# Performance work log

Hardware: AMD Instinct MI355X
Metric: run time of the kernel (lower is better)

The kernel has to match this reference:

```python
import jax, jax.numpy as jnp
import numpy as np

NUM_HEADS = 12

def setup_inputs() -> dict:
    key = jax.random.key(0)
    ks = jax.random.split(key, 6)
    B, N, C = 4, 2048, 768
    s = 0.02
    return {
        "x": jax.random.normal(ks[0], (B, N, C), jnp.float32),
        "y": jax.random.normal(ks[1], (B, N, C), jnp.float32),
        "Wq": jax.random.normal(ks[2], (C, C), jnp.float32) * s,
        "Wkv": jax.random.normal(ks[3], (2 * C, C), jnp.float32) * s,
        "tau_param": jnp.asarray(1.0, jnp.float32),
        "Wproj": jax.random.normal(ks[4], (C, C), jnp.float32) * s,
        "bproj": jnp.zeros((C,), jnp.float32),
    }

def reference(x, y, Wq, Wkv, tau_param, Wproj, bproj):
    B, N, C = x.shape
    H = NUM_HEADS
    D = C // H
    scale = D ** -0.5
    # q: [B,H,N,D]
    q = (x @ Wq.T).reshape(B, N, H, D).transpose(0, 2, 1, 3) * scale
    kv = (y @ Wkv.T).reshape(B, N, 2, H, D).transpose(2, 0, 3, 1, 4)
    k, v = kv[0], kv[1]
    tau = jax.nn.softplus(tau_param) + 1e-6
    attn = jnp.einsum("bhnd,bhmd->bhnm", q, k) / tau  # [B,H,N,N]
    attn = jax.nn.softmax(attn, axis=-1)
    out = jnp.einsum("bhnm,bhmd->bhnd", attn, v)  # [B,H,N,D]
    out = out.transpose(0, 2, 1, 3).reshape(B, N, C)
    return out @ Wproj.T + bproj
```

## Files before the change

### kernel.cpp

```cpp
#include <hip/hip_runtime.h>
#include <math.h>

typedef unsigned short u16;
typedef unsigned int u32;
typedef __fp16 fp16x2 __attribute__((ext_vector_type(2)));
typedef _Float16 half8 __attribute__((ext_vector_type(8)));
typedef float f32x4 __attribute__((ext_vector_type(4)));

#define NH   12
#define SEQ  2048
#define CDIM 768

__device__ __forceinline__ u16 f2h(float f) {
  _Float16 h = (_Float16)f;
  return __builtin_bit_cast(u16, h);
}
__device__ __forceinline__ u32 pk2(float a, float b) {
  fp16x2 h = __builtin_amdgcn_cvt_pkrtz(a, b);
  return __builtin_bit_cast(u32, h);
}
__device__ __forceinline__ void dma16(const u16* g, u16* l) {
  __builtin_amdgcn_global_load_lds(
      (const __attribute__((address_space(1))) u32*)g,
      (__attribute__((address_space(3))) u32*)l, 16, 0, 0);
}

__global__ __launch_bounds__(256) void cvt_xy(const float* __restrict__ x,
                                              const float* __restrict__ y,
                                              u16* __restrict__ xh, u16* __restrict__ yh) {
  const long NEL = 8192l * 768;
  long i = ((long)blockIdx.x * 256 + threadIdx.x) * 4;
  const float* in = (i < NEL) ? x : y;
  u16* out = (i < NEL) ? xh : yh;
  long j = (i < NEL) ? i : i - NEL;
  float4 f = *(const float4*)(in + j);
  *(uint2*)(out + j) = make_uint2(pk2(f.x, f.y), pk2(f.z, f.w));
}
__global__ __launch_bounds__(256) void cvt_w(const float* __restrict__ Wq,
                                             const float* __restrict__ Wkv,
                                             const float* __restrict__ Wp,
                                             const float* __restrict__ taup,
                                             u16* __restrict__ wqh, u16* __restrict__ wkh,
                                             u16* __restrict__ wph) {
  const long E1 = 768l * 768, E2 = E1 + 1536l * 768;
  long i = ((long)blockIdx.x * 256 + threadIdx.x) * 4;
  const float* in; u16* out; long j; float s;
  if (i < E1) {
    float t = *taup;
    float sp = (t > 20.f) ? t : log1pf(expf(t));
    s = (0.125f / (sp + 1e-6f)) * 1.44269504088896340736f;
    in = Wq; out = wqh; j = i;
  } else if (i < E2) {
    s = 1.f; in = Wkv; out = wkh; j = i - E1;
  } else {
    s = 1.f; in = Wp; out = wph; j = i - E2;
  }
  float4 f = *(const float4*)(in + j);
  *(uint2*)(out + j) = make_uint2(pk2(f.x * s, f.y * s), pk2(f.z * s, f.w * s));
}

template<int MODE, int BN, int WPB>
__global__ __launch_bounds__(256, WPB) void gemm_k(
    const u16* __restrict__ A0, const u16* __restrict__ A1,
    const u16* __restrict__ B0, const u16* __restrict__ B1,
    u16* __restrict__ oq, u16* __restrict__ ok, u16* __restrict__ ovt,
    float* __restrict__ outf, const float* __restrict__ bias)
{
  constexpr int NT = BN / 32;
  __shared__ __align__(16) u16 As[2][128 * 64];
  __shared__ __align__(16) u16 Bs[2][BN * 64];
  const int tid = threadIdx.x;
  const int wave = tid >> 6, lane = tid & 63;
  const int quad = lane >> 4, l16 = lane & 15;
  const int wr = wave >> 1, wc = wave & 1;
  const int row0 = blockIdx.x * 128;
  const int by = blockIdx.y;

  const u16* A; const u16* Bm; int cb;
  if (MODE == 0) {
    if (by < 6) { A = A0; Bm = B0; cb = by; }
    else        { A = A1; Bm = B1; cb = by - 6; }
  } else {
    A = A0; Bm = B0; cb = by;
  }
  const int col0 = cb * BN;

  const int sub = lane >> 3;
  const int csw = ((lane & 7) ^ sub) * 8;

  f32x4 acc[4][NT] = {};

  auto stage = [&](int k0, int bsel) {
    #pragma unroll
    for (int i = 0; i < 4; i++) {
      int ii = wave * 4 + i;
      dma16(A + (size_t)(row0 + ii * 8 + sub) * 768 + k0 + csw, &As[bsel][ii * 512]);
    }
    #pragma unroll
    for (int i = 0; i < BN / 32; i++) {
      int ii = wave * (BN / 32) + i;
      dma16(Bm + (size_t)(col0 + ii * 8 + sub) * 768 + k0 + csw, &Bs[bsel][ii * 512]);
    }
  };

  stage(0, 0);
  __syncthreads();

  #pragma unroll 1
  for (int t = 0; t < 12; t++) {
    const int cur = t & 1;
    if (t + 1 < 12) stage((t + 1) << 6, cur ^ 1);
    const u16* Asp = As[cur];
    const u16* Bsp = Bs[cur];
    #pragma unroll
    for (int ks = 0; ks < 2; ks++) {
      half8 af[4], bfr[NT];
      #pragma unroll
      for (int mt = 0; mt < 4; mt++)
        af[mt] = *(const half8*)&Asp[(wr * 64 + mt * 16 + l16) * 64 + (((ks * 4 + quad) ^ (l16 & 7)) * 8)];
      #pragma unroll
      for (int nt = 0; nt < NT; nt++)
        bfr[nt] = *(const half8*)&Bsp[(wc * (BN / 2) + nt * 16 + l16) * 64 + (((ks * 4 + quad) ^ (l16 & 7)) * 8)];
      #pragma unroll
      for (int mt = 0; mt < 4; mt++)
        #pragma unroll
        for (int nt = 0; nt < NT; nt++)
          acc[mt][nt] = __builtin_amdgcn_mfma_f32_16x16x32_f16(af[mt], bfr[nt], acc[mt][nt], 0, 0, 0);
    }
    __syncthreads();
  }

  #pragma unroll
  for (int mt = 0; mt < 4; mt++)
  #pragma unroll
  for (int nt = 0; nt < NT; nt++) {
    int gm0 = row0 + wr * 64 + mt * 16 + quad * 4;
    int gn = col0 + wc * (BN / 2) + nt * 16 + l16;
    f32x4 v = acc[mt][nt];
    if (MODE == 0) {
      int b = gm0 >> 11, n0 = gm0 & 2047;
      if (by < 6) {
        int h = gn >> 6, d = gn & 63;
        size_t base = (((size_t)(b * NH + h)) * SEQ + n0) * 64 + d;
        #pragma unroll
        for (int r = 0; r < 4; r++) oq[base + (size_t)r * 64] = f2h(v[r]);
      } else if (gn < CDIM) {
        int h = gn >> 6, d = gn & 63;
        size_t base = (((size_t)(b * NH + h)) * SEQ + n0) * 64 + d;
        #pragma unroll
        for (int r = 0; r < 4; r++) ok[base + (size_t)r * 64] = f2h(v[r]);
      } else {
        int c = gn - CDIM;
        int h = c >> 6, d = c & 63;
        *(uint2*)&ovt[(((size_t)(b * NH + h)) * 64 + d) * SEQ + n0] =
            make_uint2(pk2(v[0], v[1]), pk2(v[2], v[3]));
      }
    } else {
      float bv = bias[gn];
      #pragma unroll
      for (int r = 0; r < 4; r++)
        outf[(size_t)(gm0 + r) * CDIM + gn] = v[r] + bv;
    }
  }
}

__global__ __launch_bounds__(256, 3) void attn_kernel(
    const u16* __restrict__ Q, const u16* __restrict__ Kb,
    const u16* __restrict__ Vtg, u16* __restrict__ Ob)
{
  __shared__ __align__(16) u16 Ks[2][64 * 64];
  __shared__ __align__(16) u16 Vs[2][64 * 64];
  __shared__ __align__(16) u16 Ps[4 * 16 * 64];

  const int bid = (blockIdx.x & 7) * 96 + (blockIdx.x >> 3);
  const int qt = bid & 15;
  const int bh = bid >> 4;
  const int b = bh / NH, h = bh % NH;
  const u16* Qp = Q   + (size_t)bh * SEQ * 64;
  const u16* Kp = Kb  + (size_t)bh * SEQ * 64;
  const u16* Vp = Vtg + (size_t)bh * 64 * SEQ;

  const int tid = threadIdx.x;
  const int wave = tid >> 6, lane = tid & 63;
  const int quad = lane >> 4, l16 = lane & 15;
  const int sub = lane >> 3;
  const int csw = ((lane & 7) ^ sub) * 8;
  u16* Pw = Ps + wave * 16 * 64;

  half8 vone;
  #pragma unroll
  for (int j = 0; j < 8; j++) vone[j] = (_Float16)1.0f;

  half8 qf[2][2];
  #pragma unroll
  for (int mt = 0; mt < 2; mt++)
    #pragma unroll
    for (int ks = 0; ks < 2; ks++)
      qf[mt][ks] = *(const half8*)(Qp + (size_t)(qt * 128 + wave * 32 + mt * 16 + l16) * 64 + ks * 32 + quad * 8);

  f32x4 oacc[2][4] = {};
  f32x4 lacc[2] = {};

  auto stage = [&](int kt, int bsel) {
    #pragma unroll
    for (int i = 0; i < 2; i++) {
      int ii = wave * 2 + i;
      dma16(Kp + (size_t)(kt * 64 + ii * 8 + sub) * 64 + csw, &Ks[bsel][ii * 512]);
      dma16(Vp + (size_t)(ii * 8 + sub) * SEQ + kt * 64 + csw, &Vs[bsel][ii * 512]);
    }
  };

  stage(0, 0);
  __syncthreads();

  for (int kt = 0; kt < SEQ / 64; kt++) {
    const int cur = kt & 1;
    if (kt + 1 < SEQ / 64) stage(kt + 1, cur ^ 1);
    const u16* Ksp = Ks[cur];
    const u16* Vsp = Vs[cur];

    f32x4 sacc[2][4] = {};
    __builtin_amdgcn_s_setprio(1);
    #pragma unroll
    for (int ks = 0; ks < 2; ks++) {
      #pragma unroll
      for (int ntk = 0; ntk < 4; ntk++) {
        half8 kf = *(const half8*)&Ksp[(ntk * 16 + l16) * 64 + (((ks * 4 + quad) ^ (l16 & 7)) * 8)];
        #pragma unroll
        for (int mt = 0; mt < 2; mt++)
          sacc[mt][ntk] = __builtin_amdgcn_mfma_f32_16x16x32_f16(kf, qf[mt][ks], sacc[mt][ntk], 0, 0, 0);
      }
    }
    __builtin_amdgcn_s_setprio(0);

    half8 pf[2][2];
    #pragma unroll
    for (int mt = 0; mt < 2; mt++) {
      #pragma unroll
      for (int ntk = 0; ntk < 4; ntk++) {
        float p0 = __builtin_amdgcn_exp2f(sacc[mt][ntk][0]);
        float p1 = __builtin_amdgcn_exp2f(sacc[mt][ntk][1]);
        float p2 = __builtin_amdgcn_exp2f(sacc[mt][ntk][2]);
        float p3 = __builtin_amdgcn_exp2f(sacc[mt][ntk][3]);
        *(uint2*)&Pw[l16 * 64 + (((ntk * 2 + (quad >> 1)) ^ (l16 & 7)) * 8) + (quad & 1) * 4] =
            make_uint2(pk2(p0, p1), pk2(p2, p3));
      }
      pf[mt][0] = *(const half8*)&Pw[l16 * 64 + ((quad ^ (l16 & 7)) * 8)];
      pf[mt][1] = *(const half8*)&Pw[l16 * 64 + (((4 + quad) ^ (l16 & 7)) * 8)];
    }

    __builtin_amdgcn_s_setprio(1);
    #pragma unroll
    for (int ks = 0; ks < 2; ks++) {
      #pragma unroll
      for (int dt = 0; dt < 4; dt++) {
        half8 vf = *(const half8*)&Vsp[(dt * 16 + l16) * 64 + (((ks * 4 + quad) ^ (l16 & 7)) * 8)];
        #pragma unroll
        for (int mt = 0; mt < 2; mt++)
          oacc[mt][dt] = __builtin_amdgcn_mfma_f32_16x16x32_f16(pf[mt][ks], vf, oacc[mt][dt], 0, 0, 0);
      }
      #pragma unroll
      for (int mt = 0; mt < 2; mt++)
        lacc[mt] = __builtin_amdgcn_mfma_f32_16x16x32_f16(pf[mt][ks], vone, lacc[mt], 0, 0, 0);
    }
    __builtin_amdgcn_s_setprio(0);

    __syncthreads();
  }

  #pragma unroll
  for (int mt = 0; mt < 2; mt++) {
    #pragma unroll
    for (int r = 0; r < 4; r++) {
      float inv = 1.0f / lacc[mt][r];
      int n = qt * 128 + wave * 32 + mt * 16 + quad * 4 + r;
      size_t base = ((size_t)b * SEQ + n) * CDIM + h * 64;
      #pragma unroll
      for (int dt = 0; dt < 4; dt++)
        Ob[base + dt * 16 + l16] = f2h(oacc[mt][dt][r] * inv);
    }
  }
}

extern "C" void kernel_launch(void* const* d_in, const int* in_sizes, int n_in,
                              void* d_out, int out_size, void* d_ws, size_t ws_size,
                              hipStream_t stream)
{
  const float* x     = (const float*)d_in[0];
  const float* y     = (const float*)d_in[1];
  const float* Wq    = (const float*)d_in[2];
  const float* Wkv   = (const float*)d_in[3];
  const float* taup  = (const float*)d_in[4];
  const float* Wproj = (const float*)d_in[5];
  const float* bproj = (const float*)d_in[6];
  float* out = (float*)d_out;

  char* ws = (char*)d_ws;
  size_t off = 0;
  auto alloc = [&](size_t bytes) { char* p = ws + off; off += bytes; return p; };
  u16* xh  = (u16*)alloc(8192ull * 768 * 2);
  u16* yh  = (u16*)alloc(8192ull * 768 * 2);
  u16* wqh = (u16*)alloc(768ull * 768 * 2);
  u16* wkh = (u16*)alloc(1536ull * 768 * 2);
  u16* wph = (u16*)alloc(768ull * 768 * 2);
  u16* qb  = (u16*)alloc(8192ull * 768 * 2);
  u16* kb  = (u16*)alloc(8192ull * 768 * 2);
  u16* vtb = (u16*)alloc(8192ull * 768 * 2);
  u16* ao  = (u16*)alloc(8192ull * 768 * 2);

  cvt_xy<<<12288, 256, 0, stream>>>(x, y, xh, yh);
  cvt_w<<<2304, 256, 0, stream>>>(Wq, Wkv, Wproj, taup, wqh, wkh, wph);

  gemm_k<0, 128, 2><<<dim3(64, 18), 256, 0, stream>>>(xh, yh, wqh, wkh, qb, kb, vtb, nullptr, nullptr);
  attn_kernel<<<dim3(768), 256, 0, stream>>>(qb, kb, vtb, ao);
  gemm_k<2, 64, 3><<<dim3(64, 12), 256, 0, stream>>>(ao, nullptr, wph, nullptr, nullptr, nullptr, nullptr, out, bproj);
}
```

Measured before the change: 230.0 us.

## Fuse x/y fp16 conversion into QKV GEMM and software-pipeline attention PV

Removes the separate cvt_xy pass: the QKV GEMM now loads fp32 activations into registers, converts them to fp16 and writes them to LDS after the MFMA work, removing a full read/write round trip of x and y. The attention kernel is restructured into a two-stage software pipeline: QK^T for tile t overlaps with the PV product for tile t-1, and K and V loads are staged separately. This trades more register pressure and more complex scheduling for better overlap. Because the GEMM now reads fp32, its A-side global traffic doubles and it gives up the async LDS DMA.

```diff
diff --git a/kernel.cpp b/kernel.cpp
--- a/kernel.cpp
+++ b/kernel.cpp
@@ -25,17 +25,6 @@
       (__attribute__((address_space(3))) u32*)l, 16, 0, 0);
 }
 
-__global__ __launch_bounds__(256) void cvt_xy(const float* __restrict__ x,
-                                              const float* __restrict__ y,
-                                              u16* __restrict__ xh, u16* __restrict__ yh) {
-  const long NEL = 8192l * 768;
-  long i = ((long)blockIdx.x * 256 + threadIdx.x) * 4;
-  const float* in = (i < NEL) ? x : y;
-  u16* out = (i < NEL) ? xh : yh;
-  long j = (i < NEL) ? i : i - NEL;
-  float4 f = *(const float4*)(in + j);
-  *(uint2*)(out + j) = make_uint2(pk2(f.x, f.y), pk2(f.z, f.w));
-}
 __global__ __launch_bounds__(256) void cvt_w(const float* __restrict__ Wq,
                                              const float* __restrict__ Wkv,
                                              const float* __restrict__ Wp,
@@ -61,7 +50,7 @@
 
 template<int MODE, int BN, int WPB>
 __global__ __launch_bounds__(256, WPB) void gemm_k(
-    const u16* __restrict__ A0, const u16* __restrict__ A1,
+    const void* __restrict__ A0v, const void* __restrict__ A1v,
     const u16* __restrict__ B0, const u16* __restrict__ B1,
     u16* __restrict__ oq, u16* __restrict__ ok, u16* __restrict__ ovt,
     float* __restrict__ outf, const float* __restrict__ bias)
@@ -76,12 +65,15 @@
   const int row0 = blockIdx.x * 128;
   const int by = blockIdx.y;
 
-  const u16* A; const u16* Bm; int cb;
+  const float* Af;
+  const u16* Ah;
+  const u16* Bm; int cb;
   if (MODE == 0) {
-    if (by < 6) { A = A0; Bm = B0; cb = by; }
-    else        { A = A1; Bm = B1; cb = by - 6; }
+    if (by < 6) { Af = (const float*)A0v; Bm = B0; cb = by; }
+    else        { Af = (const float*)A1v; Bm = B1; cb = by - 6; }
+    Ah = nullptr;
   } else {
-    A = A0; Bm = B0; cb = by;
+    Ah = (const u16*)A0v; Bm = B0; cb = by; Af = nullptr;
   }
   const int col0 = cb * BN;
 
@@ -89,13 +81,34 @@
   const int csw = ((lane & 7) ^ sub) * 8;
 
   f32x4 acc[4][NT] = {};
-
-  auto stage = [&](int k0, int bsel) {
+  f32x4 areg[4][2];
+
+  auto stageA_load = [&](int k0) {
     #pragma unroll
     for (int i = 0; i < 4; i++) {
       int ii = wave * 4 + i;
-      dma16(A + (size_t)(row0 + ii * 8 + sub) * 768 + k0 + csw, &As[bsel][ii * 512]);
-    }
+      const float* p = Af + (size_t)(row0 + ii * 8 + sub) * 768 + k0 + csw;
+      areg[i][0] = *(const f32x4*)p;
+      areg[i][1] = *(const f32x4*)(p + 4);
+    }
+  };
+  auto stageA_write = [&](int bsel) {
+    #pragma unroll
+    for (int i = 0; i < 4; i++) {
+      int ii = wave * 4 + i;
+      uint4 w = make_uint4(pk2(areg[i][0][0], areg[i][0][1]), pk2(areg[i][0][2], areg[i][0][3]),
+                           pk2(areg[i][1][0], areg[i][1][1]), pk2(areg[i][1][2], areg[i][1][3]));
+      *(uint4*)&As[bsel][ii * 512 + lane * 8] = w;
+    }
+  };
+  auto stageA_dma = [&](int k0, int bsel) {
+    #pragma unroll
+    for (int i = 0; i < 4; i++) {
+      int ii = wave * 4 + i;
+      dma16(Ah + (size_t)(row0 + ii * 8 + sub) * 768 + k0 + csw, &As[bsel][ii * 512]);
+    }
+  };
+  auto stageB = [&](int k0, int bsel) {
     #pragma unroll
     for (int i = 0; i < BN / 32; i++) {
       int ii = wave * (BN / 32) + i;
@@ -103,13 +116,20 @@
     }
   };
 
-  stage(0, 0);
+  if (MODE == 0) { stageA_load(0); stageA_write(0); }
+  else stageA_dma(0, 0);
+  stageB(0, 0);
   __syncthreads();
 
   #pragma unroll 1
   for (int t = 0; t < 12; t++) {
     const int cur = t & 1;
-    if (t + 1 < 12) stage((t + 1) << 6, cur ^ 1);
+    const bool pre = (t + 1 < 12);
+    if (pre) {
+      if (MODE == 0) stageA_load((t + 1) << 6);
+      else stageA_dma((t + 1) << 6, cur ^ 1);
+      stageB((t + 1) << 6, cur ^ 1);
+    }
     const u16* Asp = As[cur];
     const u16* Bsp = Bs[cur];
     #pragma unroll
@@ -127,6 +147,7 @@
         for (int nt = 0; nt < NT; nt++)
           acc[mt][nt] = __builtin_amdgcn_mfma_f32_16x16x32_f16(af[mt], bfr[nt], acc[mt][nt], 0, 0, 0);
     }
+    if (MODE == 0 && pre) stageA_write(cur ^ 1);
     __syncthreads();
   }
 
@@ -200,26 +221,24 @@
 
   f32x4 oacc[2][4] = {};
   f32x4 lacc[2] = {};
-
-  auto stage = [&](int kt, int bsel) {
+  half8 pfX[2][2], pfY[2][2];
+
+  auto stageK = [&](int kt, int bsel) {
     #pragma unroll
     for (int i = 0; i < 2; i++) {
       int ii = wave * 2 + i;
       dma16(Kp + (size_t)(kt * 64 + ii * 8 + sub) * 64 + csw, &Ks[bsel][ii * 512]);
+    }
+  };
+  auto stageV = [&](int kt, int bsel) {
+    #pragma unroll
+    for (int i = 0; i < 2; i++) {
+      int ii = wave * 2 + i;
       dma16(Vp + (size_t)(ii * 8 + sub) * SEQ + kt * 64 + csw, &Vs[bsel][ii * 512]);
     }
   };
 
-  stage(0, 0);
-  __syncthreads();
-
-  for (int kt = 0; kt < SEQ / 64; kt++) {
-    const int cur = kt & 1;
-    if (kt + 1 < SEQ / 64) stage(kt + 1, cur ^ 1);
-    const u16* Ksp = Ks[cur];
-    const u16* Vsp = Vs[cur];
-
-    f32x4 sacc[2][4] = {};
+  auto qk = [&](const u16* Ksp, f32x4 (&sacc)[2][4]) {
     __builtin_amdgcn_s_setprio(1);
     #pragma unroll
     for (int ks = 0; ks < 2; ks++) {
@@ -232,8 +251,8 @@
       }
     }
     __builtin_amdgcn_s_setprio(0);
-
-    half8 pf[2][2];
+  };
+  auto softmax = [&](f32x4 (&sacc)[2][4], half8 (&pcur)[2][2]) {
     #pragma unroll
     for (int mt = 0; mt < 2; mt++) {
       #pragma unroll
@@ -245,28 +264,73 @@
         *(uint2*)&Pw[l16 * 64 + (((ntk * 2 + (quad >> 1)) ^ (l16 & 7)) * 8) + (quad & 1) * 4] =
             make_uint2(pk2(p0, p1), pk2(p2, p3));
       }
-      pf[mt][0] = *(const half8*)&Pw[l16 * 64 + ((quad ^ (l16 & 7)) * 8)];
-      pf[mt][1] = *(const half8*)&Pw[l16 * 64 + (((4 + quad) ^ (l16 & 7)) * 8)];
-    }
-
-    __builtin_amdgcn_s_setprio(1);
-    #pragma unroll
-    for (int ks = 0; ks < 2; ks++) {
+      pcur[mt][0] = *(const half8*)&Pw[l16 * 64 + ((quad ^ (l16 & 7)) * 8)];
+      pcur[mt][1] = *(const half8*)&Pw[l16 * 64 + (((4 + quad) ^ (l16 & 7)) * 8)];
+    }
+  };
+  auto pv = [&](const u16* Vsp, half8 (&pprev)[2][2]) {
+    #pragma unroll
+    for (int ks = 0; ks < 2; ks++)
       #pragma unroll
       for (int dt = 0; dt < 4; dt++) {
         half8 vf = *(const half8*)&Vsp[(dt * 16 + l16) * 64 + (((ks * 4 + quad) ^ (l16 & 7)) * 8)];
         #pragma unroll
         for (int mt = 0; mt < 2; mt++)
-          oacc[mt][dt] = __builtin_amdgcn_mfma_f32_16x16x32_f16(pf[mt][ks], vf, oacc[mt][dt], 0, 0, 0);
+          oacc[mt][dt] = __builtin_amdgcn_mfma_f32_16x16x32_f16(pprev[mt][ks], vf, oacc[mt][dt], 0, 0, 0);
       }
+  };
+  auto lsum = [&](half8 (&pcur)[2][2]) {
+    #pragma unroll
+    for (int ks = 0; ks < 2; ks++)
       #pragma unroll
       for (int mt = 0; mt < 2; mt++)
-        lacc[mt] = __builtin_amdgcn_mfma_f32_16x16x32_f16(pf[mt][ks], vone, lacc[mt], 0, 0, 0);
-    }
-    __builtin_amdgcn_s_setprio(0);
-
+        lacc[mt] = __builtin_amdgcn_mfma_f32_16x16x32_f16(pcur[mt][ks], vone, lacc[mt], 0, 0, 0);
+  };
+
+  stageK(0, 0);
+  __syncthreads();
+
+  {
+    f32x4 sacc[2][4] = {};
+    qk(Ks[0], sacc);
+    stageK(1, 1); stageV(0, 0);
+    softmax(sacc, pfX);
+    __builtin_amdgcn_s_setprio(1); lsum(pfX); __builtin_amdgcn_s_setprio(0);
     __syncthreads();
   }
+  {
+    f32x4 sacc[2][4] = {};
+    qk(Ks[1], sacc);
+    stageK(2, 0); stageV(1, 1);
+    __builtin_amdgcn_s_setprio(1); pv(Vs[0], pfX); __builtin_amdgcn_s_setprio(0);
+    softmax(sacc, pfY);
+    __builtin_amdgcn_s_setprio(1); lsum(pfY); __builtin_amdgcn_s_setprio(0);
+    __syncthreads();
+  }
+  #pragma unroll 1
+  for (int u = 1; u < 16; ++u) {
+    const int t0 = 2 * u;
+    {
+      f32x4 sacc[2][4] = {};
+      qk(Ks[0], sacc);
+      stageK(t0 + 1, 1); stageV(t0, 0);
+      __builtin_amdgcn_s_setprio(1); pv(Vs[1], pfY); __builtin_amdgcn_s_setprio(0);
+      softmax(sacc, pfX);
+      __builtin_amdgcn_s_setprio(1); lsum(pfX); __builtin_amdgcn_s_setprio(0);
+      __syncthreads();
+    }
+    {
+      f32x4 sacc[2][4] = {};
+      qk(Ks[1], sacc);
+      if (t0 + 2 < 32) stageK(t0 + 2, 0);
+      stageV(t0 + 1, 1);
+      __builtin_amdgcn_s_setprio(1); pv(Vs[0], pfX); __builtin_amdgcn_s_setprio(0);
+      softmax(sacc, pfY);
+      __builtin_amdgcn_s_setprio(1); lsum(pfY); __builtin_amdgcn_s_setprio(0);
+      __syncthreads();
+    }
+  }
+  pv(Vs[1], pfY);
 
   #pragma unroll
   for (int mt = 0; mt < 2; mt++) {
@@ -298,8 +362,6 @@
   char* ws = (char*)d_ws;
   size_t off = 0;
   auto alloc = [&](size_t bytes) { char* p = ws + off; off += bytes; return p; };
-  u16* xh  = (u16*)alloc(8192ull * 768 * 2);
-  u16* yh  = (u16*)alloc(8192ull * 768 * 2);
   u16* wqh = (u16*)alloc(768ull * 768 * 2);
   u16* wkh = (u16*)alloc(1536ull * 768 * 2);
   u16* wph = (u16*)alloc(768ull * 768 * 2);
@@ -308,10 +370,9 @@
   u16* vtb = (u16*)alloc(8192ull * 768 * 2);
   u16* ao  = (u16*)alloc(8192ull * 768 * 2);
 
-  cvt_xy<<<12288, 256, 0, stream>>>(x, y, xh, yh);
   cvt_w<<<2304, 256, 0, stream>>>(Wq, Wkv, Wproj, taup, wqh, wkh, wph);
 
-  gemm_k<0, 128, 2><<<dim3(64, 18), 256, 0, stream>>>(xh, yh, wqh, wkh, qb, kb, vtb, nullptr, nullptr);
+  gemm_k<0, 128, 2><<<dim3(64, 18), 256, 0, stream>>>(x, y, wqh, wkh, qb, kb, vtb, nullptr, nullptr);
   attn_kernel<<<dim3(768), 256, 0, stream>>>(qb, kb, vtb, ao);
   gemm_k<2, 64, 3><<<dim3(64, 12), 256, 0, stream>>>(ao, nullptr, wph, nullptr, nullptr, nullptr, nullptr, out, bproj);
 }
```

New measurement: 228.9 us. Within noise of the previous version (-0.5%).

## Fuse fp32-to-fp16 input conversion into QKV GEMM A-tile loading

Applied to the files above, without the earlier changes.

Drops the separate cvt_xy kernel and its fp16 copies of x and y. The QKV GEMM now reads fp32 A tiles straight into registers, converts them, and writes them to LDS two stages ahead. The per-iteration __syncthreads is also replaced by one explicit waitcnt-plus-barrier at the top of each loop iteration, in both the GEMM and the attention kernel. This saves a launch and a full read/write pass over x and y, but the GEMM now fetches twice as many bytes for A and needs more registers to hold the staged A data.

```diff
diff --git a/kernel.cpp b/kernel.cpp
--- a/kernel.cpp
+++ b/kernel.cpp
@@ -24,18 +24,17 @@
       (const __attribute__((address_space(1))) u32*)g,
       (__attribute__((address_space(3))) u32*)l, 16, 0, 0);
 }
-
-__global__ __launch_bounds__(256) void cvt_xy(const float* __restrict__ x,
-                                              const float* __restrict__ y,
-                                              u16* __restrict__ xh, u16* __restrict__ yh) {
-  const long NEL = 8192l * 768;
-  long i = ((long)blockIdx.x * 256 + threadIdx.x) * 4;
-  const float* in = (i < NEL) ? x : y;
-  u16* out = (i < NEL) ? xh : yh;
-  long j = (i < NEL) ? i : i - NEL;
-  float4 f = *(const float4*)(in + j);
-  *(uint2*)(out + j) = make_uint2(pk2(f.x, f.y), pk2(f.z, f.w));
-}
+__device__ __forceinline__ void publish_vm() {
+  asm volatile("s_waitcnt vmcnt(0)" ::: "memory");
+  __builtin_amdgcn_s_barrier();
+  __builtin_amdgcn_sched_barrier(0);
+}
+__device__ __forceinline__ void publish_vm_lgkm() {
+  asm volatile("s_waitcnt vmcnt(0) lgkmcnt(0)" ::: "memory");
+  __builtin_amdgcn_s_barrier();
+  __builtin_amdgcn_sched_barrier(0);
+}
+
 __global__ __launch_bounds__(256) void cvt_w(const float* __restrict__ Wq,
                                              const float* __restrict__ Wkv,
                                              const float* __restrict__ Wp,
@@ -61,7 +60,7 @@
 
 template<int MODE, int BN, int WPB>
 __global__ __launch_bounds__(256, WPB) void gemm_k(
-    const u16* __restrict__ A0, const u16* __restrict__ A1,
+    const void* __restrict__ A0v, const void* __restrict__ A1v,
     const u16* __restrict__ B0, const u16* __restrict__ B1,
     u16* __restrict__ oq, u16* __restrict__ ok, u16* __restrict__ ovt,
     float* __restrict__ outf, const float* __restrict__ bias)
@@ -76,12 +75,15 @@
   const int row0 = blockIdx.x * 128;
   const int by = blockIdx.y;
 
-  const u16* A; const u16* Bm; int cb;
+  const float* Af;
+  const u16* Ah;
+  const u16* Bm; int cb;
   if (MODE == 0) {
-    if (by < 6) { A = A0; Bm = B0; cb = by; }
-    else        { A = A1; Bm = B1; cb = by - 6; }
+    if (by < 6) { Af = (const float*)A0v; Bm = B0; cb = by; }
+    else        { Af = (const float*)A1v; Bm = B1; cb = by - 6; }
+    Ah = nullptr;
   } else {
-    A = A0; Bm = B0; cb = by;
+    Ah = (const u16*)A0v; Bm = B0; cb = by; Af = nullptr;
   }
   const int col0 = cb * BN;
 
@@ -89,45 +91,82 @@
   const int csw = ((lane & 7) ^ sub) * 8;
 
   f32x4 acc[4][NT] = {};
-
-  auto stage = [&](int k0, int bsel) {
+  f32x4 areg[4][2];
+
+  auto loadA = [&](int k0) {
     #pragma unroll
     for (int i = 0; i < 4; i++) {
       int ii = wave * 4 + i;
-      dma16(A + (size_t)(row0 + ii * 8 + sub) * 768 + k0 + csw, &As[bsel][ii * 512]);
-    }
+      const float* p = Af + (size_t)(row0 + ii * 8 + sub) * 768 + k0 + csw;
+      areg[i][0] = *(const f32x4*)p;
+      areg[i][1] = *(const f32x4*)(p + 4);
+    }
+  };
+  auto writeA = [&](int bsel) {
+    #pragma unroll
+    for (int i = 0; i < 4; i++) {
+      int ii = wave * 4 + i;
+      uint4 w = make_uint4(pk2(areg[i][0][0], areg[i][0][1]), pk2(areg[i][0][2], areg[i][0][3]),
+                           pk2(areg[i][1][0], areg[i][1][1]), pk2(areg[i][1][2], areg[i][1][3]));
+      *(uint4*)&As[bsel][ii * 512 + lane * 8] = w;
+    }
+  };
+  auto stageA_dma = [&](int k0, int bsel) {
+    #pragma unroll
+    for (int i = 0; i < 4; i++) {
+      int ii = wave * 4 + i;
+      dma16(Ah + (size_t)(row0 + ii * 8 + sub) * 768 + k0 + csw, &As[bsel][ii * 512]);
+    }
+  };
+  auto stageB = [&](int k0, int bsel) {
     #pragma unroll
     for (int i = 0; i < BN / 32; i++) {
       int ii = wave * (BN / 32) + i;
       dma16(Bm + (size_t)(col0 + ii * 8 + sub) * 768 + k0 + csw, &Bs[bsel][ii * 512]);
     }
   };
-
-  stage(0, 0);
-  __syncthreads();
+  auto compute = [&](int bsel) {
+    const u16* Asp = As[bsel];
+    const u16* Bsp = Bs[bsel];
+    #pragma unroll
+    for (int ks = 0; ks < 2; ks++) {
+      half8 af[4], bfr[NT];
+      #pragma unroll
+      for (int mt = 0; mt < 4; mt++)
+        af[mt] = *(const half8*)&Asp[(wr * 64 + mt * 16 + l16) * 64 + (((ks * 4 + quad) ^ (l16 & 7)) * 8)];
+      #pragma unroll
+      for (int nt = 0; nt < NT; nt++)
+        bfr[nt] = *(const half8*)&Bsp[(wc * (BN / 2) + nt * 16 + l16) * 64 + (((ks * 4 + quad) ^ (l16 & 7)) * 8)];
+      #pragma unroll
+      for (int mt = 0; mt < 4; mt++)
+        #pragma unroll
+        for (int nt = 0; nt < NT; nt++)
+          acc[mt][nt] = __builtin_amdgcn_mfma_f32_16x16x32_f16(af[mt], bfr[nt], acc[mt][nt], 0, 0, 0);
+    }
+  };
+
+  if (MODE == 0) {
+    stageB(0, 0);
+    loadA(0);
+    writeA(0);
+    loadA(64);
+  } else {
+    stageA_dma(0, 0);
+    stageB(0, 0);
+  }
 
   #pragma unroll 1
   for (int t = 0; t < 12; t++) {
     const int cur = t & 1;
-    if (t + 1 < 12) stage((t + 1) << 6, cur ^ 1);
-    const u16* Asp = As[cur];
-    const u16* Bsp = Bs[cur];
-    #pragma unroll
-    for (int ks = 0; ks < 2; ks++) {
-      half8 af[4], bfr[NT];
-      #pragma unroll
-      for (int mt = 0; mt < 4; mt++)
-        af[mt] = *(const half8*)&Asp[(wr * 64 + mt * 16 + l16) * 64 + (((ks * 4 + quad) ^ (l16 & 7)) * 8)];
-      #pragma unroll
-      for (int nt = 0; nt < NT; nt++)
-        bfr[nt] = *(const half8*)&Bsp[(wc * (BN / 2) + nt * 16 + l16) * 64 + (((ks * 4 + quad) ^ (l16 & 7)) * 8)];
-      #pragma unroll
-      for (int mt = 0; mt < 4; mt++)
-        #pragma unroll
-        for (int nt = 0; nt < NT; nt++)
-          acc[mt][nt] = __builtin_amdgcn_mfma_f32_16x16x32_f16(af[mt], bfr[nt], acc[mt][nt], 0, 0, 0);
-    }
-    __syncthreads();
+    if (MODE == 0) publish_vm_lgkm();
+    else           publish_vm();
+    if (t + 1 < 12) {
+      if (MODE == 0) writeA(cur ^ 1);
+      else stageA_dma((t + 1) << 6, cur ^ 1);
+      stageB((t + 1) << 6, cur ^ 1);
+    }
+    if (MODE == 0 && t + 2 < 12) loadA((t + 2) << 6);
+    compute(cur);
   }
 
   #pragma unroll
@@ -211,10 +250,11 @@
   };
 
   stage(0, 0);
-  __syncthreads();
-
+
+  #pragma unroll 1
   for (int kt = 0; kt < SEQ / 64; kt++) {
     const int cur = kt & 1;
+    publish_vm();
     if (kt + 1 < SEQ / 64) stage(kt + 1, cur ^ 1);
     const u16* Ksp = Ks[cur];
     const u16* Vsp = Vs[cur];
@@ -264,8 +304,6 @@
         lacc[mt] = __builtin_amdgcn_mfma_f32_16x16x32_f16(pf[mt][ks], vone, lacc[mt], 0, 0, 0);
     }
     __builtin_amdgcn_s_setprio(0);
-
-    __syncthreads();
   }
 
   #pragma unroll
@@ -298,8 +336,6 @@
   char* ws = (char*)d_ws;
   size_t off = 0;
   auto alloc = [&](size_t bytes) { char* p = ws + off; off += bytes; return p; };
-  u16* xh  = (u16*)alloc(8192ull * 768 * 2);
-  u16* yh  = (u16*)alloc(8192ull * 768 * 2);
   u16* wqh = (u16*)alloc(768ull * 768 * 2);
   u16* wkh = (u16*)alloc(1536ull * 768 * 2);
   u16* wph = (u16*)alloc(768ull * 768 * 2);
@@ -308,10 +344,9 @@
   u16* vtb = (u16*)alloc(8192ull * 768 * 2);
   u16* ao  = (u16*)alloc(8192ull * 768 * 2);
 
-  cvt_xy<<<12288, 256, 0, stream>>>(x, y, xh, yh);
   cvt_w<<<2304, 256, 0, stream>>>(Wq, Wkv, Wproj, taup, wqh, wkh, wph);
 
-  gemm_k<0, 128, 2><<<dim3(64, 18), 256, 0, stream>>>(xh, yh, wqh, wkh, qb, kb, vtb, nullptr, nullptr);
+  gemm_k<0, 128, 2><<<dim3(64, 18), 256, 0, stream>>>(x, y, wqh, wkh, qb, kb, vtb, nullptr, nullptr);
   attn_kernel<<<dim3(768), 256, 0, stream>>>(qb, kb, vtb, ao);
   gemm_k<2, 64, 3><<<dim3(64, 12), 256, 0, stream>>>(ao, nullptr, wph, nullptr, nullptr, nullptr, nullptr, out, bproj);
 }
```

After: 229.9 us. No clear change (-0.0%).
